# Kernel optimization log

Hardware: AMD Instinct MI355X
Metric: run time of the kernel (lower is better)

## Reference

```python
import jax, jax.numpy as jnp
import numpy as np

HEADS = 16
HEAD_DIM = 128
HIDDEN = HEADS * HEAD_DIM  # 2048
B = 4
S = 2048  # max (padded) sequence length


def setup_inputs() -> dict:
    key = jax.random.key(0)
    k1, k2, k3 = jax.random.split(key, 3)
    x = jax.random.normal(k1, (B, S, HIDDEN), dtype=jnp.float32)
    W_qkv = jax.random.normal(k2, (HIDDEN, 3 * HIDDEN), dtype=jnp.float32) * 0.02
    b_qkv = jax.random.normal(k3, (3 * HIDDEN,), dtype=jnp.float32) * 0.02
    # jagged lengths mirroring the source's TOKENS // (i + 1) pattern
    lengths = jnp.array([S // (i + 1) for i in range(B)], dtype=jnp.int64)
    return {"x": x, "W_qkv": W_qkv, "b_qkv": b_qkv, "lengths": lengths}


def reference(x, W_qkv, b_qkv, lengths):
    # x: [B, S, HIDDEN] padded jagged batch; lengths: [B] valid token counts
    qkv = x @ W_qkv + b_qkv                       # [B, S, 3*HIDDEN]
    q, k, v = jnp.split(qkv, 3, axis=-1)          # each [B, S, HIDDEN]

    def to_heads(t):  # [B, S, HIDDEN] -> [B, H, S, D]
        return t.reshape(B, S, HEADS, HEAD_DIM).transpose(0, 2, 1, 3)

    q, k, v = to_heads(q), to_heads(k), to_heads(v)

    scale = 1.0 / jnp.sqrt(jnp.asarray(HEAD_DIM, dtype=q.dtype))
    scores = jnp.einsum('bhqd,bhkd->bhqk', q, k) * scale  # [B, H, S, S]

    valid = jnp.arange(S)[None, :] < lengths[:, None]     # [B, S]
    neg = jnp.asarray(-1e30, dtype=scores.dtype)
    scores = jnp.where(valid[:, None, None, :], scores, neg)

    attn = jax.nn.softmax(scores, axis=-1)                # [B, H, S, S]
    out = jnp.einsum('bhqk,bhkd->bhqd', attn, v)          # [B, H, S, D]
    # zero out padded query rows (they don't exist in the nested tensor)
    out = out * valid[:, None, :, None].astype(out.dtype)
    return out
```

## Files before the change

kernel.cpp:

```cpp
#include <hip/hip_runtime.h>
#include <stdint.h>

#define BATCH 4
#define SEQ   2048
#define NH    16
#define HD    128
#define HID   2048
#define N3    6144

typedef _Float16 f16;
typedef _Float16 f16x8 __attribute__((ext_vector_type(8)));
typedef _Float16 f16x4 __attribute__((ext_vector_type(4)));
typedef float    f32x4 __attribute__((ext_vector_type(4)));

#define QSCALE 0.1275313895f

__device__ __forceinline__ int get_len(const int* L, int b) {
  return (L[1] == 0) ? L[2 * b] : L[b];
}

__device__ __forceinline__ void async_copy16(void* lds_uniform, const void* gptr) {
  __builtin_amdgcn_global_load_lds(
      (const __attribute__((address_space(1))) void*)(uintptr_t)gptr,
      (__attribute__((address_space(3))) void*)(uint32_t)(uintptr_t)lds_uniform,
      16, 0, 0);
}

__global__ __launch_bounds__(256) void cvt_fused(const float* __restrict__ x,
                                                 f16* __restrict__ xh,
                                                 const float* __restrict__ W,
                                                 f16* __restrict__ Wt) {
  __shared__ float tile[64][65];
  if (blockIdx.x < 8192) {
    int idx = blockIdx.x * 256 + threadIdx.x;
    int m = idx >> 8;
    int g = idx & 255;
    int p = (g & ~3) | ((g ^ ((m >> 1) & 3)) & 3);
    const float* src = x + (size_t)m * HID + g * 8;
    f16x8 o;
#pragma unroll
    for (int j = 0; j < 8; ++j) o[j] = (f16)src[j];
    *(f16x8*)&xh[(size_t)m * HID + p * 8] = o;
  } else {
    int bid = blockIdx.x - 8192;
    const int n0 = (bid % 96) * 64;
    const int k0 = (bid / 96) * 64;
    const int tid = threadIdx.x;
#pragma unroll
    for (int i = 0; i < 4; ++i) {
      int id = tid + i * 256;
      int kr = id >> 4, nc = id & 15;
      f32x4 v = *(const f32x4*)&W[(size_t)(k0 + kr) * N3 + n0 + nc * 4];
#pragma unroll
      for (int j = 0; j < 4; ++j) tile[kr][nc * 4 + j] = v[j];
    }
    __syncthreads();
#pragma unroll
    for (int i = 0; i < 2; ++i) {
      int id = tid + i * 256;
      int nl = id >> 3;
      int kc = id & 7;
      f16x8 o;
#pragma unroll
      for (int j = 0; j < 8; ++j) o[j] = (f16)tile[kc * 8 + j][nl];
      int n = n0 + nl;
      int gk = (k0 >> 3) + kc;
      int p = (gk & ~3) | ((gk ^ ((n >> 1) & 3)) & 3);
      *(f16x8*)&Wt[(size_t)n * HID + p * 8] = o;
    }
  }
}

__global__ __launch_bounds__(256, 3)
void qkv_gemm(const f16* __restrict__ xh, const f16* __restrict__ Wt,
              const float* __restrict__ bias, const int* __restrict__ lens,
              f16* __restrict__ Qh, f16* __restrict__ Kh, f16* __restrict__ Vt) {
  __shared__ f16 As[2 * 128 * 32];
  __shared__ f16 Bs[2 * 128 * 32];

  const int tid = threadIdx.x;
  const int wave = tid >> 6, lane = tid & 63;
  const int lr = lane & 15, quad = lane >> 4;
  const int nblk = blockIdx.x;
  const int mblk = blockIdx.y;
  const int m0 = mblk * 128;
  const int b = m0 >> 11;
  const int s0 = m0 & (SEQ - 1);
  const int len = get_len(lens, b);
  if (s0 >= len) return;
  const int n0 = nblk * 128;
  const int wr = (wave >> 1) * 64;
  const int wc = (wave & 1) * 64;

  f32x4 acc[4][4] = {};
  const char* xbase = (const char*)xh + (size_t)m0 * (HID * 2);
  const char* wbase = (const char*)Wt + (size_t)n0 * (HID * 2);

  for (int k0 = 0; k0 < HID; k0 += 64) {
    __syncthreads();
#pragma unroll
    for (int i = 0; i < 4; ++i) {
      int slot = wave * 4 + i;
      int hh = slot >> 3;
      int sub = slot & 7;
      int row = sub * 16 + (lane >> 2);
      size_t gcol = (size_t)k0 * 2 + hh * 64 + (lane & 3) * 16;
      async_copy16(&As[slot * 512], xbase + (size_t)row * (HID * 2) + gcol);
      async_copy16(&Bs[slot * 512], wbase + (size_t)row * (HID * 2) + gcol);
    }
    __syncthreads();

#pragma unroll
    for (int hh = 0; hh < 2; ++hh) {
      f16x8 a[4], bf[4];
#pragma unroll
      for (int mt = 0; mt < 4; ++mt) {
        int row = wr + mt * 16 + lr;
        int c = quad ^ ((row >> 1) & 3);
        a[mt] = *(const f16x8*)&As[hh * 4096 + row * 32 + c * 8];
      }
#pragma unroll
      for (int nt = 0; nt < 4; ++nt) {
        int row = wc + nt * 16 + lr;
        int c = quad ^ ((row >> 1) & 3);
        bf[nt] = *(const f16x8*)&Bs[hh * 4096 + row * 32 + c * 8];
      }
#pragma unroll
      for (int mt = 0; mt < 4; ++mt)
#pragma unroll
        for (int nt = 0; nt < 4; ++nt)
          acc[mt][nt] = __builtin_amdgcn_mfma_f32_16x16x32_f16(a[mt], bf[nt],
                                                               acc[mt][nt], 0, 0, 0);
    }
  }

  const int t = nblk >> 4;
  const int h = nblk & 15;
  const size_t bhoff = (size_t)(b * NH + h);

  if (t == 0) {
    f16* qp = Qh + bhoff * (SEQ * HD);
#pragma unroll
    for (int nt = 0; nt < 4; ++nt) {
      int d = wc + nt * 16 + lr;
      float bv = bias[n0 + d];
#pragma unroll
      for (int mt = 0; mt < 4; ++mt) {
        int sb = s0 + wr + mt * 16 + quad * 4;
#pragma unroll
        for (int r = 0; r < 4; ++r)
          qp[(size_t)(sb + r) * HD + d] = (f16)((acc[mt][nt][r] + bv) * QSCALE);
      }
    }
  } else if (t == 1) {
    f16* kp = Kh + bhoff * (SEQ * HD);
#pragma unroll
    for (int nt = 0; nt < 4; ++nt) {
      int d = wc + nt * 16 + lr;
      float bv = bias[n0 + d];
#pragma unroll
      for (int mt = 0; mt < 4; ++mt) {
        int sb = s0 + wr + mt * 16 + quad * 4;
#pragma unroll
        for (int r = 0; r < 4; ++r) {
          int s = sb + r;
          int c = (d >> 3) ^ (s & 15);
          kp[(size_t)s * HD + c * 8 + (d & 7)] = (f16)(acc[mt][nt][r] + bv);
        }
      }
    }
  } else {
    f16* vp = Vt + bhoff * (HD * SEQ);
#pragma unroll
    for (int nt = 0; nt < 4; ++nt) {
      int d = wc + nt * 16 + lr;
      float bv = bias[n0 + d];
#pragma unroll
      for (int mt = 0; mt < 4; ++mt) {
        int sb = s0 + wr + mt * 16 + quad * 4;
        f16x4 pk;
#pragma unroll
        for (int r = 0; r < 4; ++r) pk[r] = (f16)(acc[mt][nt][r] + bv);
        int p = (sb >> 3) ^ (d & 7);
        *(f16x4*)&vp[(size_t)d * SEQ + p * 8 + (sb & 7)] = pk;
      }
    }
  }
}

__global__ __launch_bounds__(512, 4)
void attn(const f16* __restrict__ Qh, const f16* __restrict__ Kh,
          const f16* __restrict__ Vt, const int* __restrict__ lens,
          float* __restrict__ out) {
  __shared__ f16 Ks[64 * 128];
  __shared__ f16 Vs[128 * 64];
  __shared__ f16 Ps[128 * 72];

  const int tid = threadIdx.x, wave = tid >> 6, lane = tid & 63;
  const int lr = lane & 15, quad = lane >> 4;
  const int id = blockIdx.x;
  const int bhlo = id & 7;
  const int r3 = id >> 3;
  const int qt = r3 & 15;
  const int bh = ((r3 >> 4) << 3) | bhlo;
  const int b = bh >> 4, h = bh & 15;
  const int len = get_len(lens, b);
  const int q0 = qt * 128;
  const size_t bho = (size_t)(b * NH + h);
  float* obase = out + bho * (size_t)(SEQ * HD);

  if (q0 >= len) {
    f32x4 z = {0.f, 0.f, 0.f, 0.f};
#pragma unroll
    for (int i = 0; i < 8; ++i) {
      int idx = tid + i * 512;
      *(f32x4*)&obase[(size_t)q0 * HD + (size_t)idx * 4] = z;
    }
    return;
  }

  f16x8 qa[4];
  {
    const f16* qp = Qh + bho * (size_t)(SEQ * HD);
    int row = q0 + wave * 16 + lr;
#pragma unroll
    for (int ks = 0; ks < 4; ++ks)
      qa[ks] = *(const f16x8*)&qp[(size_t)row * HD + ks * 32 + quad * 8];
  }

  float lrow[4] = {0.f, 0.f, 0.f, 0.f};
  f32x4 oacc[8] = {};

  const char* kpl = (const char*)(Kh + bho * (size_t)(SEQ * HD));
  const char* vpl = (const char*)(Vt + bho * (size_t)(HD * SEQ));

  const int nkt = (len + 63) >> 6;

  f16x8 kpre[2], vpre[2];
  const int kslot0 = wave * 2;
  const int kkey = (lane >> 4);
  const int kcol = (lane & 15);
  const int vdr = (lane >> 3);
  const int vcol = (lane & 7);

#pragma unroll
  for (int i = 0; i < 2; ++i) {
    int slot = kslot0 + i;
    kpre[i] = *(const f16x8*)(kpl + ((size_t)(slot * 4 + kkey) * HD + kcol * 8) * 2);
    vpre[i] = *(const f16x8*)(vpl + ((size_t)(slot * 8 + vdr) * SEQ + vcol * 8) * 2);
  }

  for (int kt = 0; kt < nkt; ++kt) {
    __syncthreads();
#pragma unroll
    for (int i = 0; i < 2; ++i) {
      int slot = kslot0 + i;
      *(f16x8*)&Ks[slot * 512 + lane * 8] = kpre[i];
      *(f16x8*)&Vs[slot * 512 + lane * 8] = vpre[i];
    }
    __syncthreads();
    if (kt + 1 < nkt) {
      size_t koff = (size_t)(kt + 1) * 64;
#pragma unroll
      for (int i = 0; i < 2; ++i) {
        int slot = kslot0 + i;
        kpre[i] = *(const f16x8*)(kpl + ((koff + slot * 4 + kkey) * HD + kcol * 8) * 2);
        vpre[i] = *(const f16x8*)(vpl + ((size_t)(slot * 8 + vdr) * SEQ + koff + vcol * 8) * 2);
      }
    }

    f32x4 sacc[4] = {};
#pragma unroll
    for (int ks = 0; ks < 4; ++ks) {
      f16x8 kb[4];
#pragma unroll
      for (int nt = 0; nt < 4; ++nt) {
        int key = nt * 16 + lr;
        int c = (ks * 4 + quad) ^ (key & 15);
        kb[nt] = *(const f16x8*)&Ks[key * 128 + c * 8];
      }
#pragma unroll
      for (int nt = 0; nt < 4; ++nt)
        sacc[nt] = __builtin_amdgcn_mfma_f32_16x16x32_f16(qa[ks], kb[nt],
                                                          sacc[nt], 0, 0, 0);
    }

    const int kbase = kt * 64;
    if (kbase + 64 > len) {
#pragma unroll
      for (int nt = 0; nt < 4; ++nt)
        if (kbase + nt * 16 + lr >= len)
#pragma unroll
          for (int r = 0; r < 4; ++r) sacc[nt][r] = -3.0e38f;
    }

#pragma unroll
    for (int nt = 0; nt < 4; ++nt)
#pragma unroll
      for (int r = 0; r < 4; ++r)
        sacc[nt][r] = __builtin_amdgcn_exp2f(sacc[nt][r]);
#pragma unroll
    for (int r = 0; r < 4; ++r)
      lrow[r] += (sacc[0][r] + sacc[1][r]) + (sacc[2][r] + sacc[3][r]);

#pragma unroll
    for (int nt = 0; nt < 4; ++nt)
#pragma unroll
      for (int r = 0; r < 4; ++r)
        Ps[(wave * 16 + quad * 4 + r) * 72 + nt * 16 + lr] = (f16)sacc[nt][r];

#pragma unroll
    for (int ks = 0; ks < 2; ++ks) {
      f16x8 pa = *(const f16x8*)&Ps[(wave * 16 + lr) * 72 + ks * 32 + quad * 8];
#pragma unroll
      for (int nt = 0; nt < 8; ++nt) {
        int d = nt * 16 + lr;
        int c = (ks * 4 + quad) ^ (d & 7);
        f16x8 vb = *(const f16x8*)&Vs[d * 64 + c * 8];
        oacc[nt] = __builtin_amdgcn_mfma_f32_16x16x32_f16(pa, vb, oacc[nt],
                                                          0, 0, 0);
      }
    }
  }

#pragma unroll
  for (int r = 0; r < 4; ++r) {
    float l = lrow[r];
    l += __shfl_xor(l, 1);
    l += __shfl_xor(l, 2);
    l += __shfl_xor(l, 4);
    l += __shfl_xor(l, 8);
    lrow[r] = 1.0f / l;
  }
  {
    int sb = q0 + wave * 16 + quad * 4;
#pragma unroll
    for (int nt = 0; nt < 8; ++nt) {
      int d = nt * 16 + lr;
#pragma unroll
      for (int r = 0; r < 4; ++r) {
        int s = sb + r;
        obase[(size_t)s * HD + d] =
            (s < len) ? oacc[nt][r] * lrow[r] : 0.0f;
      }
    }
  }
}

extern "C" void kernel_launch(void* const* d_in, const int* in_sizes, int n_in,
                              void* d_out, int out_size, void* d_ws, size_t ws_size,
                              hipStream_t stream) {
  const float* x = (const float*)d_in[0];
  const float* W = (const float*)d_in[1];
  const float* bias = (const float*)d_in[2];
  const int* lens = (const int*)d_in[3];
  float* out = (float*)d_out;

  char* ws = (char*)d_ws;
  size_t off = 0;
  f16* xh = (f16*)(ws + off); off += (size_t)BATCH * SEQ * HID * 2;
  f16* Wt = (f16*)(ws + off); off += (size_t)N3 * HID * 2;
  f16* Qh = (f16*)(ws + off); off += (size_t)BATCH * NH * SEQ * HD * 2;
  f16* Kh = (f16*)(ws + off); off += (size_t)BATCH * NH * SEQ * HD * 2;
  f16* Vt = (f16*)(ws + off); off += (size_t)BATCH * NH * SEQ * HD * 2;

  cvt_fused<<<8192 + 3072, 256, 0, stream>>>(x, xh, W, Wt);
  qkv_gemm<<<dim3(48, 64), 256, 0, stream>>>(xh, Wt, bias, lens, Qh, Kh, Vt);
  attn<<<1024, 512, 0, stream>>>(Qh, Kh, Vt, lens, out);
}
```

Measured before the change: 334.7 us.

## Rewrite QKV GEMM with 256x256 tiles, double-buffered async pipeline, swizzled grid

The QKV projection GEMM moves from 128x128 tiles with 4 waves to 256x256 tiles with 8 waves. Global-to-LDS async loads are issued in quarter-tile pieces several steps ahead into a double buffer, with vmcnt waits and barriers so loads overlap MFMA work. The block index is remapped in groups for L2 locality, and s_setprio raises priority during MFMA bursts. Each wave now holds 128 fp32 accumulators, which raises register pressure and lowers occupancy, and the larger tile makes early-exit skipping of padded rows coarser.

Result: slower. 347.9 us (+3.9%).

```diff
diff --git a/kernel.cpp b/kernel.cpp
--- a/kernel.cpp
+++ b/kernel.cpp
@@ -7,6 +7,7 @@
 #define HD    128
 #define HID   2048
 #define N3    6144
+#define NKT   32
 
 typedef _Float16 f16;
 typedef _Float16 f16x8 __attribute__((ext_vector_type(8)));
@@ -71,82 +72,118 @@
   }
 }
 
-__global__ __launch_bounds__(256, 3)
+__global__ __launch_bounds__(512, 2)
 void qkv_gemm(const f16* __restrict__ xh, const f16* __restrict__ Wt,
               const float* __restrict__ bias, const int* __restrict__ lens,
               f16* __restrict__ Qh, f16* __restrict__ Kh, f16* __restrict__ Vt) {
-  __shared__ f16 As[2 * 128 * 32];
-  __shared__ f16 Bs[2 * 128 * 32];
+  __shared__ f16 As[2][2][256 * 32];
+  __shared__ f16 Bs[2][2][256 * 32];
 
   const int tid = threadIdx.x;
   const int wave = tid >> 6, lane = tid & 63;
-  const int lr = lane & 15, quad = lane >> 4;
-  const int nblk = blockIdx.x;
-  const int mblk = blockIdx.y;
-  const int m0 = mblk * 128;
+  const int lr = lane & 15, lq = lane >> 4;
+  const int wm = wave >> 2, wn = wave & 3;
+
+  const int bid = blockIdx.x;
+  const int swz = (bid & 7) * 96 + (bid >> 3);
+  const int nblk = swz >> 5;
+  const int mblk = swz & 31;
+  const int m0 = mblk * 256;
   const int b = m0 >> 11;
   const int s0 = m0 & (SEQ - 1);
   const int len = get_len(lens, b);
   if (s0 >= len) return;
-  const int n0 = nblk * 128;
-  const int wr = (wave >> 1) * 64;
-  const int wc = (wave & 1) * 64;
-
-  f32x4 acc[4][4] = {};
+  const int n0 = nblk * 256;
+
   const char* xbase = (const char*)xh + (size_t)m0 * (HID * 2);
   const char* wbase = (const char*)Wt + (size_t)n0 * (HID * 2);
 
-  for (int k0 = 0; k0 < HID; k0 += 64) {
-    __syncthreads();
-#pragma unroll
-    for (int i = 0; i < 4; ++i) {
-      int slot = wave * 4 + i;
-      int hh = slot >> 3;
-      int sub = slot & 7;
-      int row = sub * 16 + (lane >> 2);
-      size_t gcol = (size_t)k0 * 2 + hh * 64 + (lane & 3) * 16;
-      async_copy16(&As[slot * 512], xbase + (size_t)row * (HID * 2) + gcol);
-      async_copy16(&Bs[slot * 512], wbase + (size_t)row * (HID * 2) + gcol);
-    }
-    __syncthreads();
-
-#pragma unroll
-    for (int hh = 0; hh < 2; ++hh) {
-      f16x8 a[4], bf[4];
+  auto stage_ht = [&](int hs) {
+    int kt = hs >> 2;
+    if (kt >= NKT) return;
+    int part = hs & 3;
+    int bf = kt & 1;
+    int kh = part >> 1;
+    const char* gb = (part & 1) ? wbase : xbase;
+    f16* lb = (part & 1) ? &Bs[bf][kh][0] : &As[bf][kh][0];
+    size_t gcol = (size_t)kt * 128 + kh * 64 + (lane & 3) * 16;
+    const char* src = gb + (size_t)(lane >> 2) * (HID * 2) + gcol;
+#pragma unroll
+    for (int j = 0; j < 2; ++j) {
+      int slot = wave + j * 8;
+      async_copy16(lb + slot * 512, src + (size_t)slot * 16 * (HID * 2));
+    }
+  };
+
+  f32x4 acc[8][4] = {};
+  f16x8 bfr[4];
+
+#pragma unroll
+  for (int hs = 0; hs < 6; ++hs) stage_ht(hs);
+  asm volatile("s_waitcnt vmcnt(4)" ::: "memory");
+  __builtin_amdgcn_s_barrier();
+
+#pragma unroll 1
+  for (int it = 0; it < 16; ++it) {
+#pragma unroll
+    for (int sub = 0; sub < 8; ++sub) {
+      const int bf = sub >> 2;
+      const int kk = (sub >> 1) & 1;
+      const int qd = sub & 1;
+      const f16* Ap = &As[bf][kk][0];
+      const f16* Bp = &Bs[bf][kk][0];
+      f16x8 a[4];
 #pragma unroll
       for (int mt = 0; mt < 4; ++mt) {
-        int row = wr + mt * 16 + lr;
-        int c = quad ^ ((row >> 1) & 3);
-        a[mt] = *(const f16x8*)&As[hh * 4096 + row * 32 + c * 8];
-      }
-#pragma unroll
-      for (int nt = 0; nt < 4; ++nt) {
-        int row = wc + nt * 16 + lr;
-        int c = quad ^ ((row >> 1) & 3);
-        bf[nt] = *(const f16x8*)&Bs[hh * 4096 + row * 32 + c * 8];
-      }
+        int row = wm * 128 + (qd * 4 + mt) * 16 + lr;
+        int c = lq ^ ((row >> 1) & 3);
+        a[mt] = *(const f16x8*)&Ap[row * 32 + c * 8];
+      }
+      if (qd == 0) {
+#pragma unroll
+        for (int nt = 0; nt < 4; ++nt) {
+          int row = wn * 64 + nt * 16 + lr;
+          int c = lq ^ ((row >> 1) & 3);
+          bfr[nt] = *(const f16x8*)&Bp[row * 32 + c * 8];
+        }
+      }
+      stage_ht(it * 8 + sub + 6);
+      if (qd == 1 && kk == 1) {
+        if (it == 15)
+          asm volatile("s_waitcnt vmcnt(0)" ::: "memory");
+        else
+          asm volatile("s_waitcnt vmcnt(4)" ::: "memory");
+      }
+      __builtin_amdgcn_s_barrier();
+      __builtin_amdgcn_s_setprio(1);
 #pragma unroll
       for (int mt = 0; mt < 4; ++mt)
 #pragma unroll
         for (int nt = 0; nt < 4; ++nt)
-          acc[mt][nt] = __builtin_amdgcn_mfma_f32_16x16x32_f16(a[mt], bf[nt],
-                                                               acc[mt][nt], 0, 0, 0);
-    }
-  }
-
-  const int t = nblk >> 4;
-  const int h = nblk & 15;
+          acc[qd * 4 + mt][nt] = __builtin_amdgcn_mfma_f32_16x16x32_f16(
+              a[mt], bfr[nt], acc[qd * 4 + mt][nt], 0, 0, 0);
+      __builtin_amdgcn_s_setprio(0);
+      __builtin_amdgcn_s_barrier();
+    }
+  }
+
+  const int colbase = n0 + wn * 64;
+  const int plane = colbase >> 7;
+  const int t = plane >> 4;
+  const int h = plane & 15;
+  const int dbase = colbase & 127;
+  const int srow0 = s0 + wm * 128;
   const size_t bhoff = (size_t)(b * NH + h);
 
   if (t == 0) {
     f16* qp = Qh + bhoff * (SEQ * HD);
 #pragma unroll
     for (int nt = 0; nt < 4; ++nt) {
-      int d = wc + nt * 16 + lr;
-      float bv = bias[n0 + d];
-#pragma unroll
-      for (int mt = 0; mt < 4; ++mt) {
-        int sb = s0 + wr + mt * 16 + quad * 4;
+      int d = dbase + nt * 16 + lr;
+      float bv = bias[plane * 128 + d];
+#pragma unroll
+      for (int mt = 0; mt < 8; ++mt) {
+        int sb = srow0 + mt * 16 + lq * 4;
 #pragma unroll
         for (int r = 0; r < 4; ++r)
           qp[(size_t)(sb + r) * HD + d] = (f16)((acc[mt][nt][r] + bv) * QSCALE);
@@ -156,11 +193,11 @@
     f16* kp = Kh + bhoff * (SEQ * HD);
 #pragma unroll
     for (int nt = 0; nt < 4; ++nt) {
-      int d = wc + nt * 16 + lr;
-      float bv = bias[n0 + d];
-#pragma unroll
-      for (int mt = 0; mt < 4; ++mt) {
-        int sb = s0 + wr + mt * 16 + quad * 4;
+      int d = dbase + nt * 16 + lr;
+      float bv = bias[plane * 128 + d];
+#pragma unroll
+      for (int mt = 0; mt < 8; ++mt) {
+        int sb = srow0 + mt * 16 + lq * 4;
 #pragma unroll
         for (int r = 0; r < 4; ++r) {
           int s = sb + r;
@@ -173,11 +210,11 @@
     f16* vp = Vt + bhoff * (HD * SEQ);
 #pragma unroll
     for (int nt = 0; nt < 4; ++nt) {
-      int d = wc + nt * 16 + lr;
-      float bv = bias[n0 + d];
-#pragma unroll
-      for (int mt = 0; mt < 4; ++mt) {
-        int sb = s0 + wr + mt * 16 + quad * 4;
+      int d = dbase + nt * 16 + lr;
+      float bv = bias[plane * 128 + d];
+#pragma unroll
+      for (int mt = 0; mt < 8; ++mt) {
+        int sb = srow0 + mt * 16 + lq * 4;
         f16x4 pk;
 #pragma unroll
         for (int r = 0; r < 4; ++r) pk[r] = (f16)(acc[mt][nt][r] + bv);
@@ -365,6 +402,6 @@
   f16* Vt = (f16*)(ws + off); off += (size_t)BATCH * NH * SEQ * HD * 2;
 
   cvt_fused<<<8192 + 3072, 256, 0, stream>>>(x, xh, W, Wt);
-  qkv_gemm<<<dim3(48, 64), 256, 0, stream>>>(xh, Wt, bias, lens, Qh, Kh, Vt);
+  qkv_gemm<<<768, 512, 0, stream>>>(xh, Wt, bias, lens, Qh, Kh, Vt);
   attn<<<1024, 512, 0, stream>>>(Qh, Kh, Vt, lens, out);
 }
```

## Restructure attention with transposed QK^T, register-resident P, and async LDS staging

Applied to the files above, without the earlier changes.

The attention kernel moves from 8 waves of 16 query rows each to 4 waves of 32 rows, so each K/V fragment read from LDS is reused across two row groups. It computes S^T by swapping MFMA operands, which leaves the exp'd probabilities in the layout the PV MFMA (16x16x16) needs. That removes the Ps LDS round trip and its extra shared memory. K/V tiles are now loaded with global_load_lds async copies, with explicit waitcnt/barrier staging overlapped with compute, and output stores become 16-byte vector writes. The trade-off is more registers per thread (launch bounds 256,3), fewer threads per block, and reliance on correct manual vmcnt synchronisation.

Measured after the change: 372.7 us. 11.4% more time.

```diff
diff --git a/kernel.cpp b/kernel.cpp
--- a/kernel.cpp
+++ b/kernel.cpp
@@ -188,13 +188,12 @@
   }
 }
 
-__global__ __launch_bounds__(512, 4)
+__global__ __launch_bounds__(256, 3)
 void attn(const f16* __restrict__ Qh, const f16* __restrict__ Kh,
           const f16* __restrict__ Vt, const int* __restrict__ lens,
           float* __restrict__ out) {
   __shared__ f16 Ks[64 * 128];
   __shared__ f16 Vs[128 * 64];
-  __shared__ f16 Ps[128 * 72];
 
   const int tid = threadIdx.x, wave = tid >> 6, lane = tid & 63;
   const int lr = lane & 15, quad = lane >> 4;
@@ -212,64 +211,61 @@
   if (q0 >= len) {
     f32x4 z = {0.f, 0.f, 0.f, 0.f};
 #pragma unroll
-    for (int i = 0; i < 8; ++i) {
-      int idx = tid + i * 512;
+    for (int i = 0; i < 16; ++i) {
+      int idx = tid + i * 256;
       *(f32x4*)&obase[(size_t)q0 * HD + (size_t)idx * 4] = z;
     }
     return;
   }
 
-  f16x8 qa[4];
+  f16x8 qa[2][4];
   {
     const f16* qp = Qh + bho * (size_t)(SEQ * HD);
-    int row = q0 + wave * 16 + lr;
-#pragma unroll
-    for (int ks = 0; ks < 4; ++ks)
-      qa[ks] = *(const f16x8*)&qp[(size_t)row * HD + ks * 32 + quad * 8];
-  }
-
-  float lrow[4] = {0.f, 0.f, 0.f, 0.f};
-  f32x4 oacc[8] = {};
+#pragma unroll
+    for (int rg = 0; rg < 2; ++rg) {
+      int row = q0 + wave * 32 + rg * 16 + lr;
+#pragma unroll
+      for (int ks = 0; ks < 4; ++ks)
+        qa[rg][ks] = *(const f16x8*)&qp[(size_t)row * HD + ks * 32 + quad * 8];
+    }
+  }
+
+  float lrow[2] = {0.f, 0.f};
+  f32x4 oacc[2][8] = {};
 
   const char* kpl = (const char*)(Kh + bho * (size_t)(SEQ * HD));
   const char* vpl = (const char*)(Vt + bho * (size_t)(HD * SEQ));
 
   const int nkt = (len + 63) >> 6;
 
-  f16x8 kpre[2], vpre[2];
-  const int kslot0 = wave * 2;
-  const int kkey = (lane >> 4);
-  const int kcol = (lane & 15);
-  const int vdr = (lane >> 3);
-  const int vcol = (lane & 7);
-
-#pragma unroll
-  for (int i = 0; i < 2; ++i) {
-    int slot = kslot0 + i;
-    kpre[i] = *(const f16x8*)(kpl + ((size_t)(slot * 4 + kkey) * HD + kcol * 8) * 2);
-    vpre[i] = *(const f16x8*)(vpl + ((size_t)(slot * 8 + vdr) * SEQ + vcol * 8) * 2);
-  }
+  auto stageK = [&](int kt) {
+    size_t koff = (size_t)kt * 64;
+#pragma unroll
+    for (int j = 0; j < 4; ++j) {
+      int slot = wave * 4 + j;
+      const char* src = kpl +
+          ((koff + slot * 4 + (lane >> 4)) * HD + (size_t)(lane & 15) * 8) * 2;
+      async_copy16(&Ks[slot * 512], src);
+    }
+  };
+  auto stageV = [&](int kt) {
+    size_t koff = (size_t)kt * 64;
+#pragma unroll
+    for (int j = 0; j < 4; ++j) {
+      int slot = wave * 4 + j;
+      const char* src = vpl +
+          ((size_t)(slot * 8 + (lane >> 3)) * SEQ + koff + (size_t)(lane & 7) * 8) * 2;
+      async_copy16(&Vs[slot * 512], src);
+    }
+  };
+
+  stageK(0);
+  stageV(0);
+  asm volatile("s_waitcnt vmcnt(0)" ::: "memory");
+  __builtin_amdgcn_s_barrier();
 
   for (int kt = 0; kt < nkt; ++kt) {
-    __syncthreads();
-#pragma unroll
-    for (int i = 0; i < 2; ++i) {
-      int slot = kslot0 + i;
-      *(f16x8*)&Ks[slot * 512 + lane * 8] = kpre[i];
-      *(f16x8*)&Vs[slot * 512 + lane * 8] = vpre[i];
-    }
-    __syncthreads();
-    if (kt + 1 < nkt) {
-      size_t koff = (size_t)(kt + 1) * 64;
-#pragma unroll
-      for (int i = 0; i < 2; ++i) {
-        int slot = kslot0 + i;
-        kpre[i] = *(const f16x8*)(kpl + ((koff + slot * 4 + kkey) * HD + kcol * 8) * 2);
-        vpre[i] = *(const f16x8*)(vpl + ((size_t)(slot * 8 + vdr) * SEQ + koff + vcol * 8) * 2);
-      }
-    }
-
-    f32x4 sacc[4] = {};
+    f32x4 sacc[2][4] = {};
 #pragma unroll
     for (int ks = 0; ks < 4; ++ks) {
       f16x8 kb[4];
@@ -280,69 +276,89 @@
         kb[nt] = *(const f16x8*)&Ks[key * 128 + c * 8];
       }
 #pragma unroll
-      for (int nt = 0; nt < 4; ++nt)
-        sacc[nt] = __builtin_amdgcn_mfma_f32_16x16x32_f16(qa[ks], kb[nt],
-                                                          sacc[nt], 0, 0, 0);
+      for (int nt = 0; nt < 4; ++nt) {
+        sacc[0][nt] = __builtin_amdgcn_mfma_f32_16x16x32_f16(kb[nt], qa[0][ks],
+                                                             sacc[0][nt], 0, 0, 0);
+        sacc[1][nt] = __builtin_amdgcn_mfma_f32_16x16x32_f16(kb[nt], qa[1][ks],
+                                                             sacc[1][nt], 0, 0, 0);
+      }
     }
 
     const int kbase = kt * 64;
     if (kbase + 64 > len) {
 #pragma unroll
       for (int nt = 0; nt < 4; ++nt)
-        if (kbase + nt * 16 + lr >= len)
-#pragma unroll
-          for (int r = 0; r < 4; ++r) sacc[nt][r] = -3.0e38f;
-    }
-
-#pragma unroll
-    for (int nt = 0; nt < 4; ++nt)
+#pragma unroll
+        for (int r = 0; r < 4; ++r)
+          if (kbase + nt * 16 + quad * 4 + r >= len) {
+            sacc[0][nt][r] = -3.0e38f;
+            sacc[1][nt][r] = -3.0e38f;
+          }
+    }
+
+    f16x4 pb[2][4];
+#pragma unroll
+    for (int rg = 0; rg < 2; ++rg)
+#pragma unroll
+      for (int nt = 0; nt < 4; ++nt) {
+        float e0 = __builtin_amdgcn_exp2f(sacc[rg][nt][0]);
+        float e1 = __builtin_amdgcn_exp2f(sacc[rg][nt][1]);
+        float e2 = __builtin_amdgcn_exp2f(sacc[rg][nt][2]);
+        float e3 = __builtin_amdgcn_exp2f(sacc[rg][nt][3]);
+        lrow[rg] += (e0 + e1) + (e2 + e3);
+        f16x4 pk = {(f16)e0, (f16)e1, (f16)e2, (f16)e3};
+        pb[rg][nt] = pk;
+      }
+
+    const int ktn = (kt + 1 < nkt) ? kt + 1 : nkt - 1;
+    asm volatile("s_waitcnt vmcnt(0)" ::: "memory");
+    __builtin_amdgcn_s_barrier();
+    stageK(ktn);
+
+#pragma unroll
+    for (int dt = 0; dt < 8; ++dt) {
+      int d = dt * 16 + lr;
+      f16x4 va[4];
+#pragma unroll
+      for (int nt = 0; nt < 4; ++nt) {
+        int cc = (nt * 2 + (quad >> 1)) ^ (d & 7);
+        va[nt] = *(const f16x4*)&Vs[d * 64 + cc * 8 + (quad & 1) * 4];
+      }
+#pragma unroll
+      for (int nt = 0; nt < 4; ++nt) {
+        oacc[0][dt] = __builtin_amdgcn_mfma_f32_16x16x16f16(va[nt], pb[0][nt],
+                                                            oacc[0][dt], 0, 0, 0);
+        oacc[1][dt] = __builtin_amdgcn_mfma_f32_16x16x16f16(va[nt], pb[1][nt],
+                                                            oacc[1][dt], 0, 0, 0);
+      }
+    }
+
+    __builtin_amdgcn_s_barrier();
+    stageV(ktn);
+    asm volatile("s_waitcnt vmcnt(4)" ::: "memory");
+    __builtin_amdgcn_s_barrier();
+  }
+  asm volatile("s_waitcnt vmcnt(0)" ::: "memory");
+
+  float linv[2];
+#pragma unroll
+  for (int rg = 0; rg < 2; ++rg) {
+    float l = lrow[rg];
+    l += __shfl_xor(l, 16);
+    l += __shfl_xor(l, 32);
+    linv[rg] = 1.0f / l;
+  }
+#pragma unroll
+  for (int rg = 0; rg < 2; ++rg) {
+    int s = q0 + wave * 32 + rg * 16 + lr;
+    bool valid = s < len;
+#pragma unroll
+    for (int dt = 0; dt < 8; ++dt) {
+      f32x4 o;
 #pragma unroll
       for (int r = 0; r < 4; ++r)
-        sacc[nt][r] = __builtin_amdgcn_exp2f(sacc[nt][r]);
-#pragma unroll
-    for (int r = 0; r < 4; ++r)
-      lrow[r] += (sacc[0][r] + sacc[1][r]) + (sacc[2][r] + sacc[3][r]);
-
-#pragma unroll
-    for (int nt = 0; nt < 4; ++nt)
-#pragma unroll
-      for (int r = 0; r < 4; ++r)
-        Ps[(wave * 16 + quad * 4 + r) * 72 + nt * 16 + lr] = (f16)sacc[nt][r];
-
-#pragma unroll
-    for (int ks = 0; ks < 2; ++ks) {
-      f16x8 pa = *(const f16x8*)&Ps[(wave * 16 + lr) * 72 + ks * 32 + quad * 8];
-#pragma unroll
-      for (int nt = 0; nt < 8; ++nt) {
-        int d = nt * 16 + lr;
-        int c = (ks * 4 + quad) ^ (d & 7);
-        f16x8 vb = *(const f16x8*)&Vs[d * 64 + c * 8];
-        oacc[nt] = __builtin_amdgcn_mfma_f32_16x16x32_f16(pa, vb, oacc[nt],
-                                                          0, 0, 0);
-      }
-    }
-  }
-
-#pragma unroll
-  for (int r = 0; r < 4; ++r) {
-    float l = lrow[r];
-    l += __shfl_xor(l, 1);
-    l += __shfl_xor(l, 2);
-    l += __shfl_xor(l, 4);
-    l += __shfl_xor(l, 8);
-    lrow[r] = 1.0f / l;
-  }
-  {
-    int sb = q0 + wave * 16 + quad * 4;
-#pragma unroll
-    for (int nt = 0; nt < 8; ++nt) {
-      int d = nt * 16 + lr;
-#pragma unroll
-      for (int r = 0; r < 4; ++r) {
-        int s = sb + r;
-        obase[(size_t)s * HD + d] =
-            (s < len) ? oacc[nt][r] * lrow[r] : 0.0f;
-      }
+        o[r] = valid ? oacc[rg][dt][r] * linv[rg] : 0.0f;
+      *(f32x4*)&obase[(size_t)s * HD + dt * 16 + quad * 4] = o;
     }
   }
 }
@@ -366,5 +382,5 @@
 
   cvt_fused<<<8192 + 3072, 256, 0, stream>>>(x, xh, W, Wt);
   qkv_gemm<<<dim3(48, 64), 256, 0, stream>>>(xh, Wt, bias, lens, Qh, Kh, Vt);
-  attn<<<1024, 512, 0, stream>>>(Qh, Kh, Vt, lens, out);
-}
+  attn<<<1024, 256, 0, stream>>>(Qh, Kh, Vt, lens, out);
+}
```
